# Optimization experiments

Measured on AMD Instinct MI355X. Metric: run time of the kernel, lower is better.

Reference implementation:

```python
import jax, jax.numpy as jnp
import numpy as np
from jax import lax

# ---- configuration (matches init_kwargs) ----
DH = 4.0        # grid_spacing (m)
DT = 0.0008     # time step (s), satisfies CFL for vmax=2600
PML = 20        # pml_width (cells, all four edges)
VMAX = 2600.0   # max_vel used for PML profile
PAD = 2         # halo for 4th-order (accuracy=4) stencil


def _shift(wp, k, axis, n):
    return lax.slice_in_dim(wp, PAD + k, PAD + k + n, axis=axis)


def _d1(w, axis, dh):
    # 4th-order first derivative: (-f[+2] + 8 f[+1] - 8 f[-1] + f[-2]) / (12 h)
    n = w.shape[axis]
    pad = [(0, 0)] * w.ndim
    pad[axis] = (PAD, PAD)
    wp = jnp.pad(w, pad)
    return ((_shift(wp, -2, axis, n) - _shift(wp, 2, axis, n))
            + 8.0 * (_shift(wp, 1, axis, n) - _shift(wp, -1, axis, n))) / (12.0 * dh)


def _d2(w, axis, dh):
    # 4th-order second derivative: (-f[+-2] + 16 f[+-1] - 30 f[0]) / (12 h^2)
    n = w.shape[axis]
    pad = [(0, 0)] * w.ndim
    pad[axis] = (PAD, PAD)
    wp = jnp.pad(w, pad)
    return (-(_shift(wp, -2, axis, n) + _shift(wp, 2, axis, n))
            + 16.0 * (_shift(wp, 1, axis, n) + _shift(wp, -1, axis, n))
            - 30.0 * w) / (12.0 * dh * dh)


def _pml_profiles(n, pml, dh, dt, vmax):
    # CPML absorption profiles: sigma ~ quadratic ramp into the PML,
    # b = exp(-sigma*dt), a = b - 1 (kappa=1, alpha=0)
    sigma_max = np.float32(3.0 * vmax * np.log(1000.0) / (2.0 * pml * dh))
    x = jnp.arange(n, dtype=jnp.float32)
    d = jnp.maximum(jnp.clip((pml - x) / pml, 0.0, 1.0),
                    jnp.clip((x - (n - 1 - pml)) / pml, 0.0, 1.0))
    sigma = sigma_max * d * d
    b = jnp.exp(-sigma * dt)
    return b - 1.0, b


def setup_inputs() -> dict:
    key = jax.random.key(0)
    k1, k2, k3, k4 = jax.random.split(key, 4)
    ny = nx = 400
    B, n_src, n_rec, nt = 4, 1, 100, 100
    v = 1500.0 + 1000.0 * jax.random.uniform(k1, (ny, nx), dtype=jnp.float32)
    source_amplitudes = jax.random.normal(k2, (B, n_src, nt), dtype=jnp.float32)
    source_locations = jax.random.randint(k3, (B, n_src, 2), 40, 360).astype(jnp.int64)
    receiver_locations = jax.random.randint(k4, (B, n_rec, 2), 40, 360).astype(jnp.int64)
    return {"v": v, "source_amplitudes": source_amplitudes,
            "source_locations": source_locations,
            "receiver_locations": receiver_locations}


def reference(v, source_amplitudes, source_locations, receiver_locations):
    B, n_src, nt = source_amplitudes.shape
    # replicate edge velocities into the PML region (as deepwave does)
    vp = jnp.pad(v, ((PML, PML), (PML, PML)), mode="edge")
    NY, NX = vp.shape
    v2dt2 = (vp * vp) * (DT * DT)          # [NY, NX]
    ay, by = _pml_profiles(NY, PML, DH, DT, VMAX)
    ax, bx = _pml_profiles(NX, PML, DH, DT, VMAX)
    ay, by = ay[None, :, None], by[None, :, None]
    ax, bx = ax[None, None, :], bx[None, None, :]

    sy = source_locations[..., 0] + PML    # [B, n_src]
    sx = source_locations[..., 1] + PML
    ry = receiver_locations[..., 0] + PML  # [B, n_rec]
    rx = receiver_locations[..., 1] + PML
    bidx = jnp.arange(B)[:, None]
    src_scale = v2dt2[sy, sx]              # [B, n_src]

    zero = jnp.zeros((B, NY, NX), v.dtype)
    carry0 = (zero, zero, zero, zero, zero, zero)

    def step(carry, amp_t):
        wfc, wfm, psiy, psix, zetay, zetax = carry
        # PML memory variables for first derivatives
        psiy = by * psiy + ay * _d1(wfc, 1, DH)
        psix = bx * psix + ax * _d1(wfc, 2, DH)
        # PML-corrected second derivatives
        d2y = _d2(wfc, 1, DH) + _d1(psiy, 1, DH)
        d2x = _d2(wfc, 2, DH) + _d1(psix, 2, DH)
        zetay = by * zetay + ay * d2y
        zetax = bx * zetax + ax * d2x
        # explicit leapfrog time step
        wfp = v2dt2[None] * (d2y + zetay + d2x + zetax) + 2.0 * wfc - wfm
        # inject sources scaled by v^2 dt^2 (as deepwave)
        wfp = wfp.at[bidx, sy, sx].add(src_scale * amp_t)
        rec = wfp[bidx, ry, rx]            # [B, n_rec]
        return (wfp, wfc, psiy, psix, zetay, zetax), rec

    amps_t = jnp.moveaxis(source_amplitudes, 2, 0)  # [nt, B, n_src]
    _, recs = lax.scan(step, carry0, amps_t)        # recs: [nt, B, n_rec]
    receiver_amplitudes = jnp.moveaxis(recs, 0, 2)  # [B, n_rec, nt]
    return receiver_amplitudes
```

## Files before the change

### kernel.cpp

```cpp
#include <hip/hip_runtime.h>

#define NVEL  400
#define PMLW  20
#define NSIDE 440
#define BATCH 4
#define NT    100
#define NREC  100

#define TS 55
#define GT 8
#define WP 65
#define PYP 56
#define PXP 60
#define ZP  56

#define C1f (1.0f/48.0f)
#define C2f (1.0f/192.0f)
#define NTH 1024

#define WIDX(y,x) (((y)+4)*WP + ((x)+4))

__global__ __launch_bounds__(NTH, 1) void kWave(
    const float* __restrict__ v, const float* __restrict__ amp,
    const int* __restrict__ sloc, const int* __restrict__ rloc,
    float* __restrict__ out, int* __restrict__ flags, float* __restrict__ strips)
{
    __shared__ float sWF0[63*WP], sWF1[63*WP];
    __shared__ float sPY[59*PYP];
    __shared__ float sPX[TS*PXP];
    __shared__ float sZY[TS*ZP], sZX[TS*ZP], sV2[TS*ZP];
    __shared__ float pa_y[63], pb_y[63], pa_x[63], pb_x[63];

    const int tid = threadIdx.x;
    const int bid = blockIdx.x;
    const int b   = bid >> 6;
    const int tl  = bid & 63;
    const int tyi = tl >> 3, txi = tl & 7;
    const int by0 = tyi*TS, bx0 = txi*TS;
    const int nbN = (tyi > 0)    ? bid - GT : -1;
    const int nbS = (tyi < GT-1) ? bid + GT : -1;
    const int nbW = (txi > 0)    ? bid - 1  : -1;
    const int nbE = (txi < GT-1) ? bid + 1  : -1;

    for (int i = tid; i < 63*WP; i += NTH) { sWF0[i] = 0.f; sWF1[i] = 0.f; }
    for (int i = tid; i < 59*PYP; i += NTH) sPY[i] = 0.f;
    for (int i = tid; i < TS*PXP; i += NTH) sPX[i] = 0.f;
    for (int i = tid; i < TS*ZP; i += NTH) { sZY[i] = 0.f; sZX[i] = 0.f; }
    for (int i = tid; i < TS*TS; i += NTH) {
        int y = i/TS, x = i - y*TS;
        int cy = min(max(by0 + y - PMLW, 0), NVEL-1);
        int cx = min(max(bx0 + x - PMLW, 0), NVEL-1);
        float vv = v[cy*NVEL + cx];
        sV2[y*ZP + x] = vv*vv*(float)(0.0008*0.0008);
    }
    if (tid < 63) {
        const float smax = (float)(3.0*2600.0*6.907755278982137/160.0);
        float gy = (float)(by0 + tid - 4);
        float dy = fmaxf(fminf(fmaxf((20.f-gy)/20.f,0.f),1.f),
                         fminf(fmaxf((gy-419.f)/20.f,0.f),1.f));
        float bby = expf(-smax*dy*dy*0.0008f);
        pb_y[tid] = bby; pa_y[tid] = bby - 1.f;
        float gx = (float)(bx0 + tid - 4);
        float dx = fmaxf(fminf(fmaxf((20.f-gx)/20.f,0.f),1.f),
                         fminf(fmaxf((gx-419.f)/20.f,0.f),1.f));
        float bbx = expf(-smax*dx*dx*0.0008f);
        pb_x[tid] = bbx; pa_x[tid] = bbx - 1.f;
    }

    const int sly = sloc[b*2]   + PMLW - by0;
    const int slx = sloc[b*2+1] + PMLW - bx0;

    int rofs = -1, rIdx = 0;
    if (tid < NREC) {
        int gry = rloc[(b*NREC+tid)*2]   + PMLW;
        int grx = rloc[(b*NREC+tid)*2+1] + PMLW;
        if (gry >= by0 && gry < by0+TS && grx >= bx0 && grx < bx0+TS) {
            rofs = (b*NREC+tid)*NT;
            rIdx = WIDX(gry-by0, grx-bx0);
        }
    }

    int imp_nb = -1, imp_src = 0, imp_dst = 0, exp_src = 0;
    if (tid < 880) {
        int e = tid/220, j = tid - e*220;
        if (e == 0)      { int r=j/55, c=j-55*r; imp_nb=nbN; imp_src=1*220+j; imp_dst=WIDX(r-4,c);   exp_src=WIDX(r,c); }
        else if (e == 1) { int r=j/55, c=j-55*r; imp_nb=nbS; imp_src=0*220+j; imp_dst=WIDX(55+r,c);  exp_src=WIDX(51+r,c); }
        else if (e == 2) { int r=j&3,  c=j>>2;   imp_nb=nbW; imp_src=3*220+j; imp_dst=WIDX(c,r-4);   exp_src=WIDX(c,r); }
        else             { int r=j&3,  c=j>>2;   imp_nb=nbE; imp_src=2*220+j; imp_dst=WIDX(c,55+r);  exp_src=WIDX(c,51+r); }
    }
    __syncthreads();

    float* cur = sWF0;
    float* nxt = sWF1;

#define PHASE2_BODY(yy, xx) {                                                   \
    int y = (yy), x = (xx);                                                     \
    int w = WIDX(y, x);                                                         \
    float wc = cur[w];                                                          \
    float d2y = (-(cur[w-2*WP] + cur[w+2*WP])                                   \
                 + 16.f*(cur[w-WP] + cur[w+WP]) - 30.f*wc) * C2f                \
              + (sPY[y*PYP+x] - sPY[(y+4)*PYP+x]                                \
                 + 8.f*(sPY[(y+3)*PYP+x] - sPY[(y+1)*PYP+x])) * C1f;            \
    float d2x = (-(cur[w-2] + cur[w+2])                                         \
                 + 16.f*(cur[w-1] + cur[w+1]) - 30.f*wc) * C2f                  \
              + (sPX[y*PXP+x] - sPX[y*PXP+x+4]                                  \
                 + 8.f*(sPX[y*PXP+x+3] - sPX[y*PXP+x+1])) * C1f;                \
    int zi = y*ZP + x;                                                          \
    float zy = pb_y[y+4]*sZY[zi] + pa_y[y+4]*d2y;                               \
    float zx = pb_x[x+4]*sZX[zi] + pa_x[x+4]*d2x;                               \
    sZY[zi] = zy; sZX[zi] = zx;                                                 \
    float wnew = sV2[zi]*(d2y + zy + d2x + zx) + 2.f*wc - nxt[w];               \
    if (y == sly && x == slx) wnew += sV2[zi] * amp[b*NT + t];                  \
    nxt[w] = wnew; }

    for (int t = 0; t < NT; ++t) {
        for (int i = tid; i < 51*TS; i += NTH) {
            int r = i/TS; int x = i - r*TS; r += 2;
            int w = WIDX(r, x);
            float d1 = (cur[w-2*WP] - cur[w+2*WP] + 8.f*(cur[w+WP] - cur[w-WP]))*C1f;
            int pi = (r+2)*PYP + x;
            sPY[pi] = pb_y[r+4]*sPY[pi] + pa_y[r+4]*d1;
        }
        for (int i = tid; i < 51*TS; i += NTH) {
            int y = i/51; int c = i - y*51 + 2;
            int w = WIDX(y, c);
            float d1 = (cur[w-2] - cur[w+2] + 8.f*(cur[w+1] - cur[w-1]))*C1f;
            int pi = y*PXP + c + 2;
            sPX[pi] = pb_x[c+4]*sPX[pi] + pa_x[c+4]*d1;
        }
        __syncthreads();

        for (int i = tid; i < 47*47; i += NTH) {
            int yy = i/47; int xx = i - yy*47 + 4; yy += 4;
            PHASE2_BODY(yy, xx)
        }
        if (t > 0 && imp_nb >= 0) {
            int spin = 0;
            while (__hip_atomic_load(&flags[imp_nb], __ATOMIC_RELAXED,
                                     __HIP_MEMORY_SCOPE_AGENT) < t
                   && spin < 2000000) { __builtin_amdgcn_s_sleep(1); ++spin; }
            asm volatile("" ::: "memory");
            cur[imp_dst] = __hip_atomic_load(
                &strips[(size_t)(((t-1)&1)*256 + imp_nb)*880 + imp_src],
                __ATOMIC_RELAXED, __HIP_MEMORY_SCOPE_AGENT);
        }
        __syncthreads();

        if (tid < 440) {
            int k = tid/55; int x = tid - 55*k;
            int r = (k < 4) ? (k-2) : (k+49);
            int w = WIDX(r, x);
            float d1 = (cur[w-2*WP] - cur[w+2*WP] + 8.f*(cur[w+WP] - cur[w-WP]))*C1f;
            int gy = by0 + r;
            int pi = (r+2)*PYP + x;
            float val = 0.f;
            if (gy >= 0 && gy < NSIDE) val = pb_y[r+4]*sPY[pi] + pa_y[r+4]*d1;
            sPY[pi] = val;
        } else if (tid < 880) {
            int q = tid - 440;
            int k = q/55; int y = q - 55*k;
            int c = (k < 4) ? (k-2) : (k+49);
            int w = WIDX(y, c);
            float d1 = (cur[w-2] - cur[w+2] + 8.f*(cur[w+1] - cur[w-1]))*C1f;
            int gx = bx0 + c;
            int pi = y*PXP + c + 2;
            float val = 0.f;
            if (gx >= 0 && gx < NSIDE) val = pb_x[c+4]*sPX[pi] + pa_x[c+4]*d1;
            sPX[pi] = val;
        }
        __syncthreads();

        if (tid < 816) {
            int yy, xx;
            if (tid < 440) { int k = tid/55; xx = tid - 55*k; yy = (k < 4) ? k : (k+47); }
            else { int q = tid - 440; int r8 = q >> 3; int c8 = q & 7;
                   yy = r8 + 4; xx = (c8 < 4) ? c8 : (c8+47); }
            PHASE2_BODY(yy, xx)
        }
        __syncthreads();

        if (rofs >= 0) out[rofs + t] = nxt[rIdx];
        if (t < NT-1) {
            if (tid < 880)
                __hip_atomic_store(&strips[(size_t)((t&1)*256 + bid)*880 + tid],
                                   nxt[exp_src], __ATOMIC_RELAXED,
                                   __HIP_MEMORY_SCOPE_AGENT);
            __builtin_amdgcn_s_waitcnt(0);
            __syncthreads();
            if (tid == 0)
                __hip_atomic_store(&flags[bid], t+1, __ATOMIC_RELEASE,
                                   __HIP_MEMORY_SCOPE_AGENT);
        }
        float* tmp = cur; cur = nxt; nxt = tmp;
    }
#undef PHASE2_BODY
}

extern "C" void kernel_launch(void* const* d_in, const int* in_sizes, int n_in,
                              void* d_out, int out_size, void* d_ws, size_t ws_size,
                              hipStream_t stream) {
    const float* v    = (const float*)d_in[0];
    const float* amp  = (const float*)d_in[1];
    const int*   sloc = (const int*)d_in[2];
    const int*   rloc = (const int*)d_in[3];
    float* out = (float*)d_out;

    int*   flags  = (int*)d_ws;
    float* strips = (float*)((char*)d_ws + 1024);

    hipMemsetAsync(flags, 0, 1024, stream);
    kWave<<<256, NTH, 0, stream>>>(v, amp, sloc, rloc, out, flags, strips);
}
```

Before: 746.3 us.

## Drop interior/halo overlap split; compute full tile after halo import

Removes the split where interior PML-derivative and wave updates ran before waiting on neighbor halo strips. Now each step waits for the imports first, then computes all psi and wave points of the tile in wavefront-aligned row loops (one row per 64-lane wave). It also caches the source amplitudes in shared memory. This cuts a barrier and the irregular edge-thread indexing, but gives up overlapping interior compute with the inter-block halo wait.

```diff
diff --git a/kernel.cpp b/kernel.cpp
--- a/kernel.cpp
+++ b/kernel.cpp
@@ -30,8 +30,11 @@
     __shared__ float sPX[TS*PXP];
     __shared__ float sZY[TS*ZP], sZX[TS*ZP], sV2[TS*ZP];
     __shared__ float pa_y[63], pb_y[63], pa_x[63], pb_x[63];
-
-    const int tid = threadIdx.x;
+    __shared__ float sAmp[NT];
+
+    const int tid  = threadIdx.x;
+    const int lane = tid & 63;
+    const int wrow = tid >> 6;
     const int bid = blockIdx.x;
     const int b   = bid >> 6;
     const int tl  = bid & 63;
@@ -66,6 +69,7 @@
         float bbx = expf(-smax*dx*dx*0.0008f);
         pb_x[tid] = bbx; pa_x[tid] = bbx - 1.f;
     }
+    if (tid < NT) sAmp[tid] = amp[b*NT + tid];
 
     const int sly = sloc[b*2]   + PMLW - by0;
     const int slx = sloc[b*2+1] + PMLW - bx0;
@@ -93,47 +97,7 @@
     float* cur = sWF0;
     float* nxt = sWF1;
 
-#define PHASE2_BODY(yy, xx) {                                                   \
-    int y = (yy), x = (xx);                                                     \
-    int w = WIDX(y, x);                                                         \
-    float wc = cur[w];                                                          \
-    float d2y = (-(cur[w-2*WP] + cur[w+2*WP])                                   \
-                 + 16.f*(cur[w-WP] + cur[w+WP]) - 30.f*wc) * C2f                \
-              + (sPY[y*PYP+x] - sPY[(y+4)*PYP+x]                                \
-                 + 8.f*(sPY[(y+3)*PYP+x] - sPY[(y+1)*PYP+x])) * C1f;            \
-    float d2x = (-(cur[w-2] + cur[w+2])                                         \
-                 + 16.f*(cur[w-1] + cur[w+1]) - 30.f*wc) * C2f                  \
-              + (sPX[y*PXP+x] - sPX[y*PXP+x+4]                                  \
-                 + 8.f*(sPX[y*PXP+x+3] - sPX[y*PXP+x+1])) * C1f;                \
-    int zi = y*ZP + x;                                                          \
-    float zy = pb_y[y+4]*sZY[zi] + pa_y[y+4]*d2y;                               \
-    float zx = pb_x[x+4]*sZX[zi] + pa_x[x+4]*d2x;                               \
-    sZY[zi] = zy; sZX[zi] = zx;                                                 \
-    float wnew = sV2[zi]*(d2y + zy + d2x + zx) + 2.f*wc - nxt[w];               \
-    if (y == sly && x == slx) wnew += sV2[zi] * amp[b*NT + t];                  \
-    nxt[w] = wnew; }
-
     for (int t = 0; t < NT; ++t) {
-        for (int i = tid; i < 51*TS; i += NTH) {
-            int r = i/TS; int x = i - r*TS; r += 2;
-            int w = WIDX(r, x);
-            float d1 = (cur[w-2*WP] - cur[w+2*WP] + 8.f*(cur[w+WP] - cur[w-WP]))*C1f;
-            int pi = (r+2)*PYP + x;
-            sPY[pi] = pb_y[r+4]*sPY[pi] + pa_y[r+4]*d1;
-        }
-        for (int i = tid; i < 51*TS; i += NTH) {
-            int y = i/51; int c = i - y*51 + 2;
-            int w = WIDX(y, c);
-            float d1 = (cur[w-2] - cur[w+2] + 8.f*(cur[w+1] - cur[w-1]))*C1f;
-            int pi = y*PXP + c + 2;
-            sPX[pi] = pb_x[c+4]*sPX[pi] + pa_x[c+4]*d1;
-        }
-        __syncthreads();
-
-        for (int i = tid; i < 47*47; i += NTH) {
-            int yy = i/47; int xx = i - yy*47 + 4; yy += 4;
-            PHASE2_BODY(yy, xx)
-        }
         if (t > 0 && imp_nb >= 0) {
             int spin = 0;
             while (__hip_atomic_load(&flags[imp_nb], __ATOMIC_RELAXED,
@@ -146,36 +110,63 @@
         }
         __syncthreads();
 
-        if (tid < 440) {
-            int k = tid/55; int x = tid - 55*k;
-            int r = (k < 4) ? (k-2) : (k+49);
-            int w = WIDX(r, x);
-            float d1 = (cur[w-2*WP] - cur[w+2*WP] + 8.f*(cur[w+WP] - cur[w-WP]))*C1f;
-            int gy = by0 + r;
-            int pi = (r+2)*PYP + x;
-            float val = 0.f;
-            if (gy >= 0 && gy < NSIDE) val = pb_y[r+4]*sPY[pi] + pa_y[r+4]*d1;
-            sPY[pi] = val;
-        } else if (tid < 880) {
-            int q = tid - 440;
-            int k = q/55; int y = q - 55*k;
-            int c = (k < 4) ? (k-2) : (k+49);
-            int w = WIDX(y, c);
-            float d1 = (cur[w-2] - cur[w+2] + 8.f*(cur[w+1] - cur[w-1]))*C1f;
-            int gx = bx0 + c;
-            int pi = y*PXP + c + 2;
-            float val = 0.f;
-            if (gx >= 0 && gx < NSIDE) val = pb_x[c+4]*sPX[pi] + pa_x[c+4]*d1;
-            sPX[pi] = val;
+        #pragma unroll
+        for (int k = 0; k < 4; ++k) {
+            int ri = wrow + 16*k;
+            if (ri < 59 && lane < 55) {
+                int r = ri - 2;
+                int w = WIDX(r, lane);
+                float d1 = (cur[w-2*WP] - cur[w+2*WP]
+                            + 8.f*(cur[w+WP] - cur[w-WP])) * C1f;
+                int gy = by0 + r;
+                int pi = ri*PYP + lane;
+                float val = 0.f;
+                if (gy >= 0 && gy < NSIDE)
+                    val = pb_y[r+4]*sPY[pi] + pa_y[r+4]*d1;
+                sPY[pi] = val;
+            }
+        }
+        #pragma unroll
+        for (int k = 0; k < 4; ++k) {
+            int y = wrow + 16*k;
+            if (y < 55 && lane < 59) {
+                int c = lane - 2;
+                int w = WIDX(y, c);
+                float d1 = (cur[w-2] - cur[w+2]
+                            + 8.f*(cur[w+1] - cur[w-1])) * C1f;
+                int gx = bx0 + c;
+                int pi = y*PXP + lane;
+                float val = 0.f;
+                if (gx >= 0 && gx < NSIDE)
+                    val = pb_x[c+4]*sPX[pi] + pa_x[c+4]*d1;
+                sPX[pi] = val;
+            }
         }
         __syncthreads();
 
-        if (tid < 816) {
-            int yy, xx;
-            if (tid < 440) { int k = tid/55; xx = tid - 55*k; yy = (k < 4) ? k : (k+47); }
-            else { int q = tid - 440; int r8 = q >> 3; int c8 = q & 7;
-                   yy = r8 + 4; xx = (c8 < 4) ? c8 : (c8+47); }
-            PHASE2_BODY(yy, xx)
+        #pragma unroll
+        for (int k = 0; k < 4; ++k) {
+            int y = wrow + 16*k;
+            if (y < 55 && lane < 55) {
+                int x = lane;
+                int w = WIDX(y, x);
+                float wc = cur[w];
+                float d2y = (-(cur[w-2*WP] + cur[w+2*WP])
+                             + 16.f*(cur[w-WP] + cur[w+WP]) - 30.f*wc) * C2f
+                          + (sPY[y*PYP+x] - sPY[(y+4)*PYP+x]
+                             + 8.f*(sPY[(y+3)*PYP+x] - sPY[(y+1)*PYP+x])) * C1f;
+                float d2x = (-(cur[w-2] + cur[w+2])
+                             + 16.f*(cur[w-1] + cur[w+1]) - 30.f*wc) * C2f
+                          + (sPX[y*PXP+x] - sPX[y*PXP+x+4]
+                             + 8.f*(sPX[y*PXP+x+3] - sPX[y*PXP+x+1])) * C1f;
+                int zi = y*ZP + x;
+                float zy = pb_y[y+4]*sZY[zi] + pa_y[y+4]*d2y;
+                float zx = pb_x[x+4]*sZX[zi] + pa_x[x+4]*d2x;
+                sZY[zi] = zy; sZX[zi] = zx;
+                float wnew = sV2[zi]*(d2y + zy + d2x + zx) + 2.f*wc - nxt[w];
+                if (y == sly && x == slx) wnew += sV2[zi] * sAmp[t];
+                nxt[w] = wnew;
+            }
         }
         __syncthreads();
 
@@ -193,7 +184,6 @@
         }
         float* tmp = cur; cur = nxt; nxt = tmp;
     }
-#undef PHASE2_BODY
 }
 
 extern "C" void kernel_launch(void* const* d_in, const int* in_sizes, int n_in,
```

Result: slower. 853.9 us (+14.4%).

## Overlap halo exchange with interior update using a dedicated export wavefront

Applied to the files above, without the earlier changes.

Reorders each time step so the boundary strips are computed first. One wavefront then exports halo strips to global memory and signals neighbours, while the other 15 wavefronts update the interior. The neighbour halo is loaded into a register before the PML derivative work, which hides the spin-wait latency. PML loops are remapped to a row-per-wave layout, and source amplitudes are cached in shared memory. In exchange, the interior loses one wave of compute, and the ordering of halo reads and writes becomes more delicate.

```diff
diff --git a/kernel.cpp b/kernel.cpp
--- a/kernel.cpp
+++ b/kernel.cpp
@@ -30,8 +30,11 @@
     __shared__ float sPX[TS*PXP];
     __shared__ float sZY[TS*ZP], sZX[TS*ZP], sV2[TS*ZP];
     __shared__ float pa_y[63], pb_y[63], pa_x[63], pb_x[63];
-
-    const int tid = threadIdx.x;
+    __shared__ float sAmp[NT];
+
+    const int tid  = threadIdx.x;
+    const int lane = tid & 63;
+    const int wv   = tid >> 6;
     const int bid = blockIdx.x;
     const int b   = bid >> 6;
     const int tl  = bid & 63;
@@ -66,6 +69,7 @@
         float bbx = expf(-smax*dx*dx*0.0008f);
         pb_x[tid] = bbx; pa_x[tid] = bbx - 1.f;
     }
+    if (tid < NT) sAmp[tid] = amp[b*NT + tid];
 
     const int sly = sloc[b*2]   + PMLW - by0;
     const int slx = sloc[b*2+1] + PMLW - bx0;
@@ -80,13 +84,13 @@
         }
     }
 
-    int imp_nb = -1, imp_src = 0, imp_dst = 0, exp_src = 0;
+    int imp_nb = -1, imp_src = 0, imp_dst = 0;
     if (tid < 880) {
         int e = tid/220, j = tid - e*220;
-        if (e == 0)      { int r=j/55, c=j-55*r; imp_nb=nbN; imp_src=1*220+j; imp_dst=WIDX(r-4,c);   exp_src=WIDX(r,c); }
-        else if (e == 1) { int r=j/55, c=j-55*r; imp_nb=nbS; imp_src=0*220+j; imp_dst=WIDX(55+r,c);  exp_src=WIDX(51+r,c); }
-        else if (e == 2) { int r=j&3,  c=j>>2;   imp_nb=nbW; imp_src=3*220+j; imp_dst=WIDX(c,r-4);   exp_src=WIDX(c,r); }
-        else             { int r=j&3,  c=j>>2;   imp_nb=nbE; imp_src=2*220+j; imp_dst=WIDX(c,55+r);  exp_src=WIDX(c,51+r); }
+        if (e == 0)      { int r=j/55, c=j-55*r; imp_nb=nbN; imp_src=1*220+j; imp_dst=WIDX(r-4,c); }
+        else if (e == 1) { int r=j/55, c=j-55*r; imp_nb=nbS; imp_src=0*220+j; imp_dst=WIDX(55+r,c); }
+        else if (e == 2) { int r=j&3,  c=j>>2;   imp_nb=nbW; imp_src=3*220+j; imp_dst=WIDX(c,r-4); }
+        else             { int r=j&3,  c=j>>2;   imp_nb=nbE; imp_src=2*220+j; imp_dst=WIDX(c,55+r); }
     }
     __syncthreads();
 
@@ -110,63 +114,74 @@
     float zx = pb_x[x+4]*sZX[zi] + pa_x[x+4]*d2x;                               \
     sZY[zi] = zy; sZX[zi] = zx;                                                 \
     float wnew = sV2[zi]*(d2y + zy + d2x + zx) + 2.f*wc - nxt[w];               \
-    if (y == sly && x == slx) wnew += sV2[zi] * amp[b*NT + t];                  \
+    if (y == sly && x == slx) wnew += sV2[zi] * sAmp[t];                        \
     nxt[w] = wnew; }
 
     for (int t = 0; t < NT; ++t) {
-        for (int i = tid; i < 51*TS; i += NTH) {
-            int r = i/TS; int x = i - r*TS; r += 2;
-            int w = WIDX(r, x);
-            float d1 = (cur[w-2*WP] - cur[w+2*WP] + 8.f*(cur[w+WP] - cur[w-WP]))*C1f;
-            int pi = (r+2)*PYP + x;
-            sPY[pi] = pb_y[r+4]*sPY[pi] + pa_y[r+4]*d1;
-        }
-        for (int i = tid; i < 51*TS; i += NTH) {
-            int y = i/51; int c = i - y*51 + 2;
-            int w = WIDX(y, c);
-            float d1 = (cur[w-2] - cur[w+2] + 8.f*(cur[w+1] - cur[w-1]))*C1f;
-            int pi = y*PXP + c + 2;
-            sPX[pi] = pb_x[c+4]*sPX[pi] + pa_x[c+4]*d1;
-        }
-        __syncthreads();
-
-        for (int i = tid; i < 47*47; i += NTH) {
-            int yy = i/47; int xx = i - yy*47 + 4; yy += 4;
-            PHASE2_BODY(yy, xx)
-        }
+        float hval = 0.f;
         if (t > 0 && imp_nb >= 0) {
             int spin = 0;
             while (__hip_atomic_load(&flags[imp_nb], __ATOMIC_RELAXED,
                                      __HIP_MEMORY_SCOPE_AGENT) < t
                    && spin < 2000000) { __builtin_amdgcn_s_sleep(1); ++spin; }
-            asm volatile("" ::: "memory");
-            cur[imp_dst] = __hip_atomic_load(
+            hval = __hip_atomic_load(
                 &strips[(size_t)(((t-1)&1)*256 + imp_nb)*880 + imp_src],
                 __ATOMIC_RELAXED, __HIP_MEMORY_SCOPE_AGENT);
         }
-        __syncthreads();
-
-        if (tid < 440) {
-            int k = tid/55; int x = tid - 55*k;
-            int r = (k < 4) ? (k-2) : (k+49);
-            int w = WIDX(r, x);
-            float d1 = (cur[w-2*WP] - cur[w+2*WP] + 8.f*(cur[w+WP] - cur[w-WP]))*C1f;
-            int gy = by0 + r;
-            int pi = (r+2)*PYP + x;
-            float val = 0.f;
-            if (gy >= 0 && gy < NSIDE) val = pb_y[r+4]*sPY[pi] + pa_y[r+4]*d1;
-            sPY[pi] = val;
-        } else if (tid < 880) {
-            int q = tid - 440;
-            int k = q/55; int y = q - 55*k;
-            int c = (k < 4) ? (k-2) : (k+49);
-            int w = WIDX(y, c);
-            float d1 = (cur[w-2] - cur[w+2] + 8.f*(cur[w+1] - cur[w-1]))*C1f;
-            int gx = bx0 + c;
-            int pi = y*PXP + c + 2;
-            float val = 0.f;
-            if (gx >= 0 && gx < NSIDE) val = pb_x[c+4]*sPX[pi] + pa_x[c+4]*d1;
-            sPX[pi] = val;
+        asm volatile("" ::: "memory");
+
+        #pragma unroll
+        for (int k = 0; k < 4; ++k) {
+            int r = 2 + wv + 16*k;
+            if (r <= 52 && lane < 55) {
+                int w = WIDX(r, lane);
+                float d1 = (cur[w-2*WP] - cur[w+2*WP]
+                            + 8.f*(cur[w+WP] - cur[w-WP])) * C1f;
+                int pi = (r+2)*PYP + lane;
+                sPY[pi] = pb_y[r+4]*sPY[pi] + pa_y[r+4]*d1;
+            }
+        }
+        #pragma unroll
+        for (int k = 0; k < 4; ++k) {
+            int y = wv + 16*k;
+            if (y < 55 && lane < 51) {
+                int c = lane + 2;
+                int w = WIDX(y, c);
+                float d1 = (cur[w-2] - cur[w+2]
+                            + 8.f*(cur[w+1] - cur[w-1])) * C1f;
+                int pi = y*PXP + c + 2;
+                sPX[pi] = pb_x[c+4]*sPX[pi] + pa_x[c+4]*d1;
+            }
+        }
+
+        if (t > 0 && imp_nb >= 0) cur[imp_dst] = hval;
+        __syncthreads();
+
+        if (wv < 8) {
+            int r = (wv < 4) ? wv-2 : wv+49;
+            if (lane < 55) {
+                int w = WIDX(r, lane);
+                float d1 = (cur[w-2*WP] - cur[w+2*WP]
+                            + 8.f*(cur[w+WP] - cur[w-WP])) * C1f;
+                int gy = by0 + r;
+                int pi = (r+2)*PYP + lane;
+                float val = 0.f;
+                if (gy >= 0 && gy < NSIDE) val = pb_y[r+4]*sPY[pi] + pa_y[r+4]*d1;
+                sPY[pi] = val;
+            }
+        } else {
+            int c = (wv < 12) ? wv-10 : wv+41;
+            if (lane < 55) {
+                int y = lane;
+                int w = WIDX(y, c);
+                float d1 = (cur[w-2] - cur[w+2]
+                            + 8.f*(cur[w+1] - cur[w-1])) * C1f;
+                int gx = bx0 + c;
+                int pi = y*PXP + c + 2;
+                float val = 0.f;
+                if (gx >= 0 && gx < NSIDE) val = pb_x[c+4]*sPX[pi] + pa_x[c+4]*d1;
+                sPX[pi] = val;
+            }
         }
         __syncthreads();
 
@@ -179,18 +194,54 @@
         }
         __syncthreads();
 
+        if (wv == 15) {
+            if (t < NT-1) {
+                float ev[14];
+                #pragma unroll
+                for (int k = 0; k < 14; ++k) {
+                    int i = lane + 64*k;
+                    if (i < 880) {
+                        int e = (i>=660)?3:(i>=440)?2:(i>=220)?1:0;
+                        int j = i - 220*e;
+                        int src;
+                        if (e < 2) {
+                            int r = (j>=165)+(j>=110)+(j>=55);
+                            int c = j - 55*r;
+                            src = (e==0) ? WIDX(r,c) : WIDX(51+r,c);
+                        } else {
+                            int r = j & 3, c = j >> 2;
+                            src = (e==2) ? WIDX(c,r) : WIDX(c,51+r);
+                        }
+                        ev[k] = nxt[src];
+                    }
+                }
+                #pragma unroll
+                for (int k = 0; k < 14; ++k) {
+                    int i = lane + 64*k;
+                    if (i < 880)
+                        __hip_atomic_store(
+                            &strips[(size_t)((t&1)*256 + bid)*880 + i], ev[k],
+                            __ATOMIC_RELAXED, __HIP_MEMORY_SCOPE_AGENT);
+                }
+                __builtin_amdgcn_s_waitcnt(0);
+                if (lane == 0)
+                    __hip_atomic_store(&flags[bid], t+1, __ATOMIC_RELEASE,
+                                       __HIP_MEMORY_SCOPE_AGENT);
+            }
+        } else {
+            #pragma unroll
+            for (int k = 0; k < 3; ++k) {
+                int idx = tid + 960*k;
+                if (idx < 2209) {
+                    int yy = idx/47, xx = idx - 47*yy;
+                    PHASE2_BODY(yy+4, xx+4)
+                }
+            }
+        }
+        __syncthreads();
+
         if (rofs >= 0) out[rofs + t] = nxt[rIdx];
-        if (t < NT-1) {
-            if (tid < 880)
-                __hip_atomic_store(&strips[(size_t)((t&1)*256 + bid)*880 + tid],
-                                   nxt[exp_src], __ATOMIC_RELAXED,
-                                   __HIP_MEMORY_SCOPE_AGENT);
-            __builtin_amdgcn_s_waitcnt(0);
-            __syncthreads();
-            if (tid == 0)
-                __hip_atomic_store(&flags[bid], t+1, __ATOMIC_RELEASE,
-                                   __HIP_MEMORY_SCOPE_AGENT);
-        }
+
         float* tmp = cur; cur = nxt; nxt = tmp;
     }
 #undef PHASE2_BODY
```

After: 767.2 us. +2.8%, slower.
